# Kernel tuning notes

Hardware: AMD Instinct MI355X
Metric: run time of the kernel (lower is better)

Reference implementation:

```python
import jax, jax.numpy as jnp
import numpy as np
import math

NH = 12  # num_attention_heads (multiple of 4 required by pattern dispatch)


def _forward(Input, hidden_states, attention_mask, Wq, bq, Wk, bk, Wv, bv, Wo, bo, L):
    b, n, _, H = Input.shape
    hd = H // NH
    G = NH // 4  # heads per criss-cross pattern
    # boolean-mask gather of valid (head, tail) entity pairs, row-major like torch
    bi, ri, ci = jnp.nonzero(attention_mask > 0, size=L)
    x = Input[bi, ri, ci]            # [L, H] keys/values source
    xq = hidden_states[bi, ri, ci]   # [L, H] query source
    q = (xq @ Wq + bq).reshape(L, NH, hd)
    k = (x @ Wk + bk).reshape(L, NH, hd)
    v = (x @ Wv + bv).reshape(L, NH, hd)
    ar = jnp.arange(n)
    # per-pattern criss-cross masks for query position (b, r, c), each [L, n]
    m0 = attention_mask[bi, ri, :] * (ar[None, :] != ci[:, None])  # row r, exclude self col c
    m1 = attention_mask[bi, :, ci] * (ar[None, :] != ri[:, None])  # col c, exclude self row r
    m2 = attention_mask[bi, :, ri]                                  # col r (no self exclusion)
    m3 = attention_mask[bi, ci, :]                                  # row c (no self exclusion)
    adds = jnp.stack([(1.0 - m) * -10000.0 for m in (m0, m1, m2, m3)], axis=1)  # [L, 4, n]
    # scatter per-pattern head groups into zero grid, then criss-cross gather
    k_gs, v_gs = [], []
    for p in range(4):
        sk = jnp.zeros((b, n, n, G, hd), k.dtype).at[bi, ri, ci].set(k[:, p::4])
        sv = jnp.zeros((b, n, n, G, hd), v.dtype).at[bi, ri, ci].set(v[:, p::4])
        if p == 0:
            gk, gv = sk[bi, ri], sv[bi, ri]          # element [l,k] = grid[b, r, k]
        elif p == 1:
            gk, gv = sk[bi, :, ci], sv[bi, :, ci]    # grid[b, k, c]
        elif p == 2:
            gk, gv = sk[bi, :, ri], sv[bi, :, ri]    # grid[b, k, r]
        else:
            gk, gv = sk[bi, ci], sv[bi, ci]          # grid[b, c, k]
        k_gs.append(gk)
        v_gs.append(gv)
    kg = jnp.stack(k_gs, axis=1)  # [L, 4, n, G, hd]
    vg = jnp.stack(v_gs, axis=1)
    # head h = 4*g + p (k[:, p::4] picks heads p, p+4, p+8)
    kg = kg.transpose(0, 3, 1, 2, 4).reshape(L, NH, n, hd)
    vg = vg.transpose(0, 3, 1, 2, 4).reshape(L, NH, n, hd)
    amask = jnp.broadcast_to(adds[:, None, :, :], (L, G, 4, n)).reshape(L, NH, n)
    # prepend self key/value; NOTE: original code uses additive bias +1.0 (ones) for the self slot
    kf = jnp.concatenate([k[:, :, None, :], kg], axis=2)   # [L, NH, n+1, hd]
    vf = jnp.concatenate([v[:, :, None, :], vg], axis=2)
    amask = jnp.concatenate([jnp.ones((L, NH, 1), amask.dtype), amask], axis=-1)
    scores = jnp.einsum('lhd,lhkd->lhk', q, kf) / math.sqrt(hd) + amask
    probs = jax.nn.softmax(scores, axis=-1)  # dropout is identity in eval
    ctx = jnp.einsum('lhk,lhkd->lhd', probs, vf).reshape(L, H)
    return ctx @ Wo + bo


def setup_inputs() -> dict:
    key = jax.random.key(0)
    ks = jax.random.split(key, 8)
    b, n, H = 2, 40, 768
    Input = jax.random.normal(ks[0], (b, n, n, H), jnp.float32)
    hidden_states = jax.random.normal(ks[1], (b, n, n, H), jnp.float32)
    # all valid entity pairs except self pairs -> deterministic L
    attention_mask = (jnp.ones((b, n, n)) - jnp.eye(n)[None]).astype(jnp.float32)
    L = int(b * n * (n - 1))  # 3120
    std = 0.02
    Wq = std * jax.random.normal(ks[2], (H, H), jnp.float32)
    Wk = std * jax.random.normal(ks[3], (H, H), jnp.float32)
    Wv = std * jax.random.normal(ks[4], (H, H), jnp.float32)
    Wo = std * jax.random.normal(ks[5], (H, H), jnp.float32)
    bq = jnp.zeros((H,), jnp.float32)
    bk = jnp.zeros((H,), jnp.float32)
    bv = jnp.zeros((H,), jnp.float32)
    bo = jnp.zeros((H,), jnp.float32)
    return {"Input": Input, "hidden_states": hidden_states, "attention_mask": attention_mask,
            "Wq": Wq, "bq": bq, "Wk": Wk, "bk": bk, "Wv": Wv, "bv": bv, "Wo": Wo, "bo": bo, "L": L}


def reference(Input, hidden_states, attention_mask, Wq, bq, Wk, bk, Wv, bv, Wo, bo, L):
    return _forward(Input, hidden_states, attention_mask, Wq, bq, Wk, bk, Wv, bv, Wo, bo, L)
```

## Files before the change

### kernel.cpp

```cpp
#include <hip/hip_runtime.h>
#include <hip/hip_bf16.h>
#include <math.h>

#define NHEADS 12

typedef __attribute__((ext_vector_type(4))) float f32x4;
typedef __attribute__((ext_vector_type(8))) short bf16x8;

__device__ __forceinline__ unsigned short f2bf(float x) {
  __hip_bfloat16 h = __float2bfloat16(x);
  return *reinterpret_cast<unsigned short*>(&h);
}
__device__ __forceinline__ float bf2f(unsigned short u) {
  union { unsigned int i; float f; } c; c.i = ((unsigned int)u) << 16; return c.f;
}

__global__ __launch_bounds__(1024) void build_idx(const float* __restrict__ mask,
                                                  int total,
                                                  int* __restrict__ pos2l,
                                                  int* __restrict__ lidx,
                                                  const float* __restrict__ bk,
                                                  const float* __restrict__ bv,
                                                  float* __restrict__ bkv,
                                                  int H) {
  __shared__ int cnt[1024];
  int t = threadIdx.x;
  if (t < H) { bkv[t] = bk[t]; bkv[H + t] = bv[t]; }
  int per = (total + 1023) >> 10;
  int begin = t * per;
  int end = begin + per; if (end > total) end = total;
  if (begin > total) begin = total;
  int c = 0;
  for (int i = begin; i < end; ++i) c += (mask[i] > 0.f) ? 1 : 0;
  cnt[t] = c;
  __syncthreads();
  for (int off = 1; off < 1024; off <<= 1) {
    int vv = (t >= off) ? cnt[t - off] : 0;
    __syncthreads();
    cnt[t] += vv;
    __syncthreads();
  }
  int excl = cnt[t] - c;
  for (int i = begin; i < end; ++i) {
    if (mask[i] > 0.f) { pos2l[i] = excl; lidx[excl] = i; ++excl; }
    else pos2l[i] = -1;
  }
}

__global__ __launch_bounds__(256) void wconv(const float* __restrict__ W0, const float* __restrict__ W1,
                                             const float* __restrict__ W2, const float* __restrict__ W3,
                                             unsigned short* __restrict__ T0, unsigned short* __restrict__ T1,
                                             unsigned short* __restrict__ T2, unsigned short* __restrict__ T3,
                                             int H) {
  const float* W = (blockIdx.z == 0) ? W0 : (blockIdx.z == 1) ? W1 : (blockIdx.z == 2) ? W2 : W3;
  unsigned short* T = (blockIdx.z == 0) ? T0 : (blockIdx.z == 1) ? T1 : (blockIdx.z == 2) ? T2 : T3;
  __shared__ float tile[32][33];
  int k0 = blockIdx.y * 32, n0 = blockIdx.x * 32;
  int t = threadIdx.x;
  int kk = t >> 3, n4 = (t & 7) * 4;
  float4 v = *reinterpret_cast<const float4*>(W + (size_t)(k0 + kk) * H + n0 + n4);
  tile[n4 + 0][kk] = v.x; tile[n4 + 1][kk] = v.y; tile[n4 + 2][kk] = v.z; tile[n4 + 3][kk] = v.w;
  __syncthreads();
  int nn2 = t >> 3, k4 = (t & 7) * 4;
#pragma unroll
  for (int e = 0; e < 4; ++e)
    T[(size_t)(n0 + nn2) * H + k0 + k4 + e] = f2bf(tile[nn2][k4 + e]);
}

__global__ __launch_bounds__(256) void gatherconv(const float* __restrict__ hidden,
                                                  const float* __restrict__ input,
                                                  const int* __restrict__ lidx,
                                                  unsigned short* __restrict__ Aq,
                                                  unsigned short* __restrict__ Akv,
                                                  int L, int H) {
  int i = blockIdx.x * 256 + threadIdx.x;
  int per = H / 8;
  if (i >= L * per) return;
  int row = i / per;
  int sub = (i - row * per) * 8;
  size_t src = (size_t)lidx[row] * H + sub;
  size_t dst = (size_t)row * H + sub;
  {
    float4 a = *reinterpret_cast<const float4*>(hidden + src);
    float4 b = *reinterpret_cast<const float4*>(hidden + src + 4);
    bf16x8 st;
    st[0]=f2bf(a.x); st[1]=f2bf(a.y); st[2]=f2bf(a.z); st[3]=f2bf(a.w);
    st[4]=f2bf(b.x); st[5]=f2bf(b.y); st[6]=f2bf(b.z); st[7]=f2bf(b.w);
    *reinterpret_cast<bf16x8*>(Aq + dst) = st;
  }
  {
    float4 a = *reinterpret_cast<const float4*>(input + src);
    float4 b = *reinterpret_cast<const float4*>(input + src + 4);
    bf16x8 st;
    st[0]=f2bf(a.x); st[1]=f2bf(a.y); st[2]=f2bf(a.z); st[3]=f2bf(a.w);
    st[4]=f2bf(b.x); st[5]=f2bf(b.y); st[6]=f2bf(b.z); st[7]=f2bf(b.w);
    *reinterpret_cast<bf16x8*>(Akv + dst) = st;
  }
}

#define GBM 128
#define GBN 64
#define GBK 64

template <bool OUT_BF16>
__global__ __launch_bounds__(256) void gemm_bf16(const unsigned short* __restrict__ A,
                                                 const unsigned short* __restrict__ Bt,
                                                 const float* __restrict__ bias,
                                                 void* __restrict__ C,
                                                 int M, int N, int K) {
  __shared__ unsigned short sA[GBM * GBK];
  __shared__ unsigned short sB[GBN * GBK];
  int tid = threadIdx.x;
  int wid = tid >> 6, lane = tid & 63;
  int wm = wid >> 1, wn = wid & 1;
  int m0 = blockIdx.y * GBM, n0 = blockIdx.x * GBN;
  int lr = lane & 15, lq = lane >> 4;
  f32x4 acc[4][2] = {};

  for (int k0 = 0; k0 < K; k0 += GBK) {
#pragma unroll
    for (int r = 0; r < 4; ++r) {
      int c = (r * 4 + wid) * 64 + lane;
      int row = c >> 3, sl = c & 7;
      int sg = sl ^ (row & 7);
      const unsigned short* g = A + (size_t)(m0 + row) * K + k0 + sg * 8;
      __builtin_amdgcn_global_load_lds((const __attribute__((address_space(1))) unsigned int*)g,
                                       (__attribute__((address_space(3))) unsigned int*)(sA + (size_t)(r * 4 + wid) * 512),
                                       16, 0, 0);
    }
#pragma unroll
    for (int r = 0; r < 2; ++r) {
      int c = (r * 4 + wid) * 64 + lane;
      int row = c >> 3, sl = c & 7;
      int sg = sl ^ (row & 7);
      const unsigned short* g = Bt + (size_t)(n0 + row) * K + k0 + sg * 8;
      __builtin_amdgcn_global_load_lds((const __attribute__((address_space(1))) unsigned int*)g,
                                       (__attribute__((address_space(3))) unsigned int*)(sB + (size_t)(r * 4 + wid) * 512),
                                       16, 0, 0);
    }
    __syncthreads();
#pragma unroll
    for (int ks = 0; ks < 2; ++ks) {
      bf16x8 af[4], bfr[2];
#pragma unroll
      for (int i = 0; i < 4; ++i) {
        int row = wm * 64 + i * 16 + lr;
        int slot = (ks * 4 + lq) ^ (row & 7);
        af[i] = *reinterpret_cast<const bf16x8*>(sA + row * 64 + slot * 8);
      }
#pragma unroll
      for (int j = 0; j < 2; ++j) {
        int rn = wn * 32 + j * 16 + lr;
        int slot = (ks * 4 + lq) ^ (rn & 7);
        bfr[j] = *reinterpret_cast<const bf16x8*>(sB + rn * 64 + slot * 8);
      }
#pragma unroll
      for (int i = 0; i < 4; ++i)
#pragma unroll
        for (int j = 0; j < 2; ++j)
          acc[i][j] = __builtin_amdgcn_mfma_f32_16x16x32_bf16(af[i], bfr[j], acc[i][j], 0, 0, 0);
    }
    __syncthreads();
  }

#pragma unroll
  for (int i = 0; i < 4; ++i) {
#pragma unroll
    for (int j = 0; j < 2; ++j) {
      int gcol = n0 + wn * 32 + j * 16 + lr;
      float bv = bias[gcol];
      int rbase = m0 + wm * 64 + i * 16 + lq * 4;
#pragma unroll
      for (int r = 0; r < 4; ++r) {
        int gm = rbase + r;
        if (gm >= M) continue;
        float val = acc[i][j][r] + bv;
        if (OUT_BF16) ((unsigned short*)C)[(size_t)gm * N + gcol] = f2bf(val);
        else          ((float*)C)[(size_t)gm * N + gcol] = val;
      }
    }
  }
}

__global__ __launch_bounds__(128) void attn3(const unsigned short* __restrict__ qb,
                                             const unsigned short* __restrict__ KVb,
                                             const float* __restrict__ mask,
                                             const int* __restrict__ pos2l,
                                             unsigned short* __restrict__ ctx,
                                             int n, int H) {
  __shared__ unsigned short Ks[40 * 72];
  __shared__ unsigned short Vs[40 * 72];
  __shared__ float S[40][42];
  __shared__ float mrow[40];
  __shared__ int qlist[40];

  int bx = blockIdx.x;
  int r0 = bx % n;
  int h3 = (bx / n) % 3;
  int p = (bx / (3 * n)) % 4;
  int bi = bx / (12 * n);
  int h = p + 4 * h3;
  int nn = n * n;
  bool rowkeys = (p == 0 || p == 3);
  bool rowq = (p == 0 || p == 2);
  bool excl = (p < 2);
  int t = threadIdx.x;
  int H2 = 2 * H;

  if (t < 80) {
    int half = t / 40, j = t % 40;
    int keypos = rowkeys ? (r0 * n + j) : (j * n + r0);
    int l2 = pos2l[bi * nn + keypos];
    unsigned short* dst = (half ? Vs : Ks) + j * 72;
    if (l2 >= 0) {
      const unsigned short* src = KVb + (size_t)l2 * H2 + half * H + h * 64;
#pragma unroll
      for (int e8 = 0; e8 < 8; ++e8)
        *reinterpret_cast<bf16x8*>(dst + e8 * 8) = *reinterpret_cast<const bf16x8*>(src + e8 * 8);
    } else {
      bf16x8 z = {};
#pragma unroll
      for (int e8 = 0; e8 < 8; ++e8) *reinterpret_cast<bf16x8*>(dst + e8 * 8) = z;
    }
  }
  if (t < 40) {
    mrow[t] = rowkeys ? mask[bi * nn + r0 * n + t] : mask[bi * nn + t * n + r0];
    int qpos = rowq ? (r0 * n + t) : (t * n + r0);
    qlist[t] = pos2l[bi * nn + qpos];
  }
  __syncthreads();

  int c = t % 40;
  int role = t / 40;
  int lq = (t < 80) ? qlist[c] : -1;

  if (lq >= 0) {
    float qf[64];
    const unsigned short* qp = qb + (size_t)lq * H + h * 64;
#pragma unroll
    for (int e8 = 0; e8 < 8; ++e8) {
      bf16x8 t8 = *reinterpret_cast<const bf16x8*>(qp + e8 * 8);
#pragma unroll
      for (int e = 0; e < 8; ++e) qf[e8 * 8 + e] = bf2f((unsigned short)t8[e]);
    }
    int j0 = role * 20;
#pragma unroll 2
    for (int j = j0; j < j0 + 20; ++j) {
      float acc = 0.f;
#pragma unroll
      for (int e8 = 0; e8 < 8; ++e8) {
        bf16x8 kv = *reinterpret_cast<const bf16x8*>(Ks + j * 72 + e8 * 8);
#pragma unroll
        for (int e = 0; e < 8; ++e) acc = fmaf(qf[e8 * 8 + e], bf2f((unsigned short)kv[e]), acc);
      }
      float mval = mrow[j] * ((excl && j == c) ? 0.f : 1.f);
      S[c][j] = acc * 0.125f + (1.f - mval) * -10000.f;
    }
    if (role == 0) {
      const unsigned short* kp = KVb + (size_t)lq * H2 + h * 64;
      float acc = 0.f;
#pragma unroll
      for (int e8 = 0; e8 < 8; ++e8) {
        bf16x8 kv = *reinterpret_cast<const bf16x8*>(kp + e8 * 8);
#pragma unroll
        for (int e = 0; e < 8; ++e) acc = fmaf(qf[e8 * 8 + e], bf2f((unsigned short)kv[e]), acc);
      }
      S[c][40] = acc * 0.125f + 1.0f;
    }
  }
  __syncthreads();

  if (t < 40 && qlist[t] >= 0) {
    float mx = -3.0e38f;
    for (int j = 0; j <= 40; ++j) mx = fmaxf(mx, S[t][j]);
    float sum = 0.f;
    for (int j = 0; j <= 40; ++j) { float e = __expf(S[t][j] - mx); S[t][j] = e; sum += e; }
    float inv = 1.f / sum;
    for (int j = 0; j <= 40; ++j) S[t][j] *= inv;
  }
  __syncthreads();

  if (lq >= 0) {
    int d0 = role * 32;
    const unsigned short* vsp = KVb + (size_t)lq * H2 + H + h * 64 + d0;
    float pself = S[c][40];
#pragma unroll
    for (int ch = 0; ch < 4; ++ch) {
      int dd = d0 + ch * 8;
      float facc[8];
      bf16x8 vself = *reinterpret_cast<const bf16x8*>(vsp + ch * 8);
#pragma unroll
      for (int e = 0; e < 8; ++e) facc[e] = pself * bf2f((unsigned short)vself[e]);
      for (int j = 0; j < 40; ++j) {
        float pj = S[c][j];
        bf16x8 vv = *reinterpret_cast<const bf16x8*>(Vs + j * 72 + dd);
#pragma unroll
        for (int e = 0; e < 8; ++e) facc[e] = fmaf(pj, bf2f((unsigned short)vv[e]), facc[e]);
      }
      bf16x8 st;
#pragma unroll
      for (int e = 0; e < 8; ++e) st[e] = f2bf(facc[e]);
      *reinterpret_cast<bf16x8*>(ctx + (size_t)lq * H + h * 64 + dd) = st;
    }
  }
}

extern "C" void kernel_launch(void* const* d_in, const int* in_sizes, int n_in,
                              void* d_out, int out_size, void* d_ws, size_t ws_size,
                              hipStream_t stream) {
  const float* Input  = (const float*)d_in[0];
  const float* hidden = (const float*)d_in[1];
  const float* mask   = (const float*)d_in[2];
  const float* Wq = (const float*)d_in[3];
  const float* bq = (const float*)d_in[4];
  const float* Wk = (const float*)d_in[5];
  const float* bk = (const float*)d_in[6];
  const float* Wv = (const float*)d_in[7];
  const float* bv = (const float*)d_in[8];
  const float* Wo = (const float*)d_in[9];
  const float* bo = (const float*)d_in[10];

  int H = (int)llround(sqrt((double)in_sizes[3]));
  int total = in_sizes[2];
  int L = out_size / H;
  int bn = total - L;
  int n = total / bn;
  int b = bn / n;
  int mtiles = (L + GBM - 1) / GBM;
  int Mpad = mtiles * GBM;
  size_t aElems = (size_t)Mpad * H;

  char* p = (char*)d_ws;
  auto take = [&](size_t bytes) { char* r = p; p += (bytes + 255) & ~(size_t)255; return r; };
  int* lidx  = (int*)take((size_t)L * 4);
  int* pos2l = (int*)take((size_t)total * 4);
  float* bkv = (float*)take((size_t)2 * H * 4);
  unsigned short* Wqt  = (unsigned short*)take((size_t)H * H * 2);
  unsigned short* Wot  = (unsigned short*)take((size_t)H * H * 2);
  unsigned short* Wkvt = (unsigned short*)take((size_t)2 * H * H * 2);
  unsigned short* Aq   = (unsigned short*)take(aElems * 2);
  unsigned short* Akv  = (unsigned short*)take(aElems * 2);
  unsigned short* qb2  = (unsigned short*)take(aElems * 2);
  unsigned short* KVb  = (unsigned short*)take(aElems * 2 * 2);
  unsigned short* ctxb = (unsigned short*)take(aElems * 2);

  build_idx<<<1, 1024, 0, stream>>>(mask, total, pos2l, lidx, bk, bv, bkv, H);
  wconv<<<dim3(H / 32, H / 32, 4), 256, 0, stream>>>(Wq, Wk, Wv, Wo, Wqt, Wkvt, Wkvt + (size_t)H * H, Wot, H);
  {
    int nthr = L * (H / 8);
    gatherconv<<<(nthr + 255) / 256, 256, 0, stream>>>(hidden, Input, lidx, Aq, Akv, L, H);
  }
  gemm_bf16<true><<<dim3(H / GBN, mtiles), 256, 0, stream>>>(Aq,  Wqt,  bq,  qb2, L, H,     H);
  gemm_bf16<true><<<dim3(2 * H / GBN, mtiles), 256, 0, stream>>>(Akv, Wkvt, bkv, KVb, L, 2 * H, H);
  attn3<<<b * 4 * 3 * n, 128, 0, stream>>>(qb2, KVb, mask, pos2l, ctxb, n, H);
  gemm_bf16<false><<<dim3(H / GBN, mtiles), 256, 0, stream>>>(ctxb, Wot, bo, (float*)d_out, L, H, H);
}
```

Baseline: 96.69 us.

## Merge prep kernels, fuse Q and KV GEMMs, double-buffer GEMM LDS staging

Folds the index-build and weight-conversion kernels into one launch, with a single trailing block doing the mask scan on 256 threads instead of 1024. The Q and KV projections are merged into one GEMM launch that picks its operands by block index. The GEMM core now double-buffers LDS so the next K tile is loaded while MFMAs run on the current one, dropping one barrier per iteration. This cuts launch count and hides global-load latency, at the cost of twice the LDS per block (possibly lower occupancy) and a slower serial scan in the prep block.

```diff
diff --git a/kernel.cpp b/kernel.cpp
--- a/kernel.cpp
+++ b/kernel.cpp
@@ -15,56 +15,59 @@
   union { unsigned int i; float f; } c; c.i = ((unsigned int)u) << 16; return c.f;
 }
 
-__global__ __launch_bounds__(1024) void build_idx(const float* __restrict__ mask,
-                                                  int total,
-                                                  int* __restrict__ pos2l,
-                                                  int* __restrict__ lidx,
-                                                  const float* __restrict__ bk,
-                                                  const float* __restrict__ bv,
-                                                  float* __restrict__ bkv,
-                                                  int H) {
-  __shared__ int cnt[1024];
+__global__ __launch_bounds__(256) void prep(const float* __restrict__ mask, int total,
+                                            int* __restrict__ pos2l, int* __restrict__ lidx,
+                                            const float* __restrict__ bk, const float* __restrict__ bv,
+                                            float* __restrict__ bkv,
+                                            const float* __restrict__ W0, const float* __restrict__ W1,
+                                            const float* __restrict__ W2, const float* __restrict__ W3,
+                                            unsigned short* __restrict__ T0, unsigned short* __restrict__ T1,
+                                            unsigned short* __restrict__ T2, unsigned short* __restrict__ T3,
+                                            int H) {
+  int nt32 = H / 32;
+  int nw = nt32 * nt32 * 4;
+  int bx = blockIdx.x;
   int t = threadIdx.x;
-  if (t < H) { bkv[t] = bk[t]; bkv[H + t] = bv[t]; }
-  int per = (total + 1023) >> 10;
-  int begin = t * per;
-  int end = begin + per; if (end > total) end = total;
-  if (begin > total) begin = total;
-  int c = 0;
-  for (int i = begin; i < end; ++i) c += (mask[i] > 0.f) ? 1 : 0;
-  cnt[t] = c;
-  __syncthreads();
-  for (int off = 1; off < 1024; off <<= 1) {
-    int vv = (t >= off) ? cnt[t - off] : 0;
+  if (bx < nw) {
+    __shared__ float tile[32][33];
+    int z = bx / (nt32 * nt32);
+    int rem = bx - z * nt32 * nt32;
+    int byy = rem / nt32;
+    int bxx = rem - byy * nt32;
+    const float* W = (z == 0) ? W0 : (z == 1) ? W1 : (z == 2) ? W2 : W3;
+    unsigned short* T = (z == 0) ? T0 : (z == 1) ? T1 : (z == 2) ? T2 : T3;
+    int k0 = byy * 32, n0 = bxx * 32;
+    int kk = t >> 3, n4 = (t & 7) * 4;
+    float4 v = *reinterpret_cast<const float4*>(W + (size_t)(k0 + kk) * H + n0 + n4);
+    tile[n4 + 0][kk] = v.x; tile[n4 + 1][kk] = v.y; tile[n4 + 2][kk] = v.z; tile[n4 + 3][kk] = v.w;
     __syncthreads();
-    cnt[t] += vv;
+    int nn2 = t >> 3, k4 = (t & 7) * 4;
+#pragma unroll
+    for (int e = 0; e < 4; ++e)
+      T[(size_t)(n0 + nn2) * H + k0 + k4 + e] = f2bf(tile[nn2][k4 + e]);
+  } else {
+    __shared__ int cnt[256];
+    for (int i = t; i < H; i += 256) { bkv[i] = bk[i]; bkv[H + i] = bv[i]; }
+    int per = (total + 255) >> 8;
+    int begin = t * per;
+    int end = begin + per; if (end > total) end = total;
+    if (begin > total) begin = total;
+    int c = 0;
+    for (int i = begin; i < end; ++i) c += (mask[i] > 0.f) ? 1 : 0;
+    cnt[t] = c;
     __syncthreads();
-  }
-  int excl = cnt[t] - c;
-  for (int i = begin; i < end; ++i) {
-    if (mask[i] > 0.f) { pos2l[i] = excl; lidx[excl] = i; ++excl; }
-    else pos2l[i] = -1;
-  }
-}
-
-__global__ __launch_bounds__(256) void wconv(const float* __restrict__ W0, const float* __restrict__ W1,
-                                             const float* __restrict__ W2, const float* __restrict__ W3,
-                                             unsigned short* __restrict__ T0, unsigned short* __restrict__ T1,
-                                             unsigned short* __restrict__ T2, unsigned short* __restrict__ T3,
-                                             int H) {
-  const float* W = (blockIdx.z == 0) ? W0 : (blockIdx.z == 1) ? W1 : (blockIdx.z == 2) ? W2 : W3;
-  unsigned short* T = (blockIdx.z == 0) ? T0 : (blockIdx.z == 1) ? T1 : (blockIdx.z == 2) ? T2 : T3;
-  __shared__ float tile[32][33];
-  int k0 = blockIdx.y * 32, n0 = blockIdx.x * 32;
-  int t = threadIdx.x;
-  int kk = t >> 3, n4 = (t & 7) * 4;
-  float4 v = *reinterpret_cast<const float4*>(W + (size_t)(k0 + kk) * H + n0 + n4);
-  tile[n4 + 0][kk] = v.x; tile[n4 + 1][kk] = v.y; tile[n4 + 2][kk] = v.z; tile[n4 + 3][kk] = v.w;
-  __syncthreads();
-  int nn2 = t >> 3, k4 = (t & 7) * 4;
-#pragma unroll
-  for (int e = 0; e < 4; ++e)
-    T[(size_t)(n0 + nn2) * H + k0 + k4 + e] = f2bf(tile[nn2][k4 + e]);
+    for (int off = 1; off < 256; off <<= 1) {
+      int vv = (t >= off) ? cnt[t - off] : 0;
+      __syncthreads();
+      cnt[t] += vv;
+      __syncthreads();
+    }
+    int excl = cnt[t] - c;
+    for (int i = begin; i < end; ++i) {
+      if (mask[i] > 0.f) { pos2l[i] = excl; lidx[excl] = i; ++excl; }
+      else pos2l[i] = -1;
+    }
+  }
 }
 
 __global__ __launch_bounds__(256) void gatherconv(const float* __restrict__ hidden,
@@ -103,21 +106,19 @@
 #define GBK 64
 
 template <bool OUT_BF16>
-__global__ __launch_bounds__(256) void gemm_bf16(const unsigned short* __restrict__ A,
-                                                 const unsigned short* __restrict__ Bt,
-                                                 const float* __restrict__ bias,
-                                                 void* __restrict__ C,
-                                                 int M, int N, int K) {
-  __shared__ unsigned short sA[GBM * GBK];
-  __shared__ unsigned short sB[GBN * GBK];
+__device__ __forceinline__ void gemm_core(const unsigned short* __restrict__ A,
+                                          const unsigned short* __restrict__ Bt,
+                                          const float* __restrict__ bias,
+                                          void* __restrict__ C,
+                                          int M, int N, int K, int m0, int n0,
+                                          unsigned short* sA, unsigned short* sB) {
   int tid = threadIdx.x;
   int wid = tid >> 6, lane = tid & 63;
   int wm = wid >> 1, wn = wid & 1;
-  int m0 = blockIdx.y * GBM, n0 = blockIdx.x * GBN;
   int lr = lane & 15, lq = lane >> 4;
   f32x4 acc[4][2] = {};
 
-  for (int k0 = 0; k0 < K; k0 += GBK) {
+  auto STAGE = [&](int buf, int k0) {
 #pragma unroll
     for (int r = 0; r < 4; ++r) {
       int c = (r * 4 + wid) * 64 + lane;
@@ -125,7 +126,7 @@
       int sg = sl ^ (row & 7);
       const unsigned short* g = A + (size_t)(m0 + row) * K + k0 + sg * 8;
       __builtin_amdgcn_global_load_lds((const __attribute__((address_space(1))) unsigned int*)g,
-                                       (__attribute__((address_space(3))) unsigned int*)(sA + (size_t)(r * 4 + wid) * 512),
+                                       (__attribute__((address_space(3))) unsigned int*)(sA + buf * (GBM * GBK) + (r * 4 + wid) * 512),
                                        16, 0, 0);
     }
 #pragma unroll
@@ -135,10 +136,19 @@
       int sg = sl ^ (row & 7);
       const unsigned short* g = Bt + (size_t)(n0 + row) * K + k0 + sg * 8;
       __builtin_amdgcn_global_load_lds((const __attribute__((address_space(1))) unsigned int*)g,
-                                       (__attribute__((address_space(3))) unsigned int*)(sB + (size_t)(r * 4 + wid) * 512),
+                                       (__attribute__((address_space(3))) unsigned int*)(sB + buf * (GBN * GBK) + (r * 4 + wid) * 512),
                                        16, 0, 0);
     }
+  };
+
+  const int nt = K / GBK;
+  STAGE(0, 0);
+  int cur = 0;
+  for (int t = 0; t < nt; ++t) {
     __syncthreads();
+    if (t + 1 < nt) STAGE(cur ^ 1, (t + 1) * GBK);
+    const unsigned short* pA = sA + cur * (GBM * GBK);
+    const unsigned short* pB = sB + cur * (GBN * GBK);
 #pragma unroll
     for (int ks = 0; ks < 2; ++ks) {
       bf16x8 af[4], bfr[2];
@@ -146,13 +156,13 @@
       for (int i = 0; i < 4; ++i) {
         int row = wm * 64 + i * 16 + lr;
         int slot = (ks * 4 + lq) ^ (row & 7);
-        af[i] = *reinterpret_cast<const bf16x8*>(sA + row * 64 + slot * 8);
+        af[i] = *reinterpret_cast<const bf16x8*>(pA + row * 64 + slot * 8);
       }
 #pragma unroll
       for (int j = 0; j < 2; ++j) {
         int rn = wn * 32 + j * 16 + lr;
         int slot = (ks * 4 + lq) ^ (rn & 7);
-        bfr[j] = *reinterpret_cast<const bf16x8*>(sB + rn * 64 + slot * 8);
+        bfr[j] = *reinterpret_cast<const bf16x8*>(pB + rn * 64 + slot * 8);
       }
 #pragma unroll
       for (int i = 0; i < 4; ++i)
@@ -160,7 +170,7 @@
         for (int j = 0; j < 2; ++j)
           acc[i][j] = __builtin_amdgcn_mfma_f32_16x16x32_bf16(af[i], bfr[j], acc[i][j], 0, 0, 0);
     }
-    __syncthreads();
+    cur ^= 1;
   }
 
 #pragma unroll
@@ -180,6 +190,36 @@
       }
     }
   }
+}
+
+__global__ __launch_bounds__(256) void gemm_qkv(const unsigned short* __restrict__ Aq,
+                                                const unsigned short* __restrict__ Akv,
+                                                const unsigned short* __restrict__ Wqt,
+                                                const unsigned short* __restrict__ Wkvt,
+                                                const float* __restrict__ bq,
+                                                const float* __restrict__ bkv,
+                                                unsigned short* __restrict__ Cq,
+                                                unsigned short* __restrict__ Ckv,
+                                                int M, int K, int H) {
+  __shared__ unsigned short sA[2 * GBM * GBK];
+  __shared__ unsigned short sB[2 * GBN * GBK];
+  int nq = H / GBN;
+  int bx = blockIdx.x;
+  int m0 = blockIdx.y * GBM;
+  if (bx < nq)
+    gemm_core<true>(Aq, Wqt, bq, Cq, M, H, K, m0, bx * GBN, sA, sB);
+  else
+    gemm_core<true>(Akv, Wkvt, bkv, Ckv, M, 2 * H, K, m0, (bx - nq) * GBN, sA, sB);
+}
+
+__global__ __launch_bounds__(256) void gemm_out(const unsigned short* __restrict__ A,
+                                                const unsigned short* __restrict__ Bt,
+                                                const float* __restrict__ bias,
+                                                float* __restrict__ C,
+                                                int M, int N, int K) {
+  __shared__ unsigned short sA[2 * GBM * GBK];
+  __shared__ unsigned short sB[2 * GBN * GBK];
+  gemm_core<false>(A, Bt, bias, C, M, N, K, blockIdx.y * GBM, blockIdx.x * GBN, sA, sB);
 }
 
 __global__ __launch_bounds__(128) void attn3(const unsigned short* __restrict__ qb,
@@ -344,14 +384,17 @@
   unsigned short* KVb  = (unsigned short*)take(aElems * 2 * 2);
   unsigned short* ctxb = (unsigned short*)take(aElems * 2);
 
-  build_idx<<<1, 1024, 0, stream>>>(mask, total, pos2l, lidx, bk, bv, bkv, H);
-  wconv<<<dim3(H / 32, H / 32, 4), 256, 0, stream>>>(Wq, Wk, Wv, Wo, Wqt, Wkvt, Wkvt + (size_t)H * H, Wot, H);
+  int nt32 = H / 32;
+  int nwconv = nt32 * nt32 * 4;
+  prep<<<nwconv + 1, 256, 0, stream>>>(mask, total, pos2l, lidx, bk, bv, bkv,
+                                       Wq, Wk, Wv, Wo,
+                                       Wqt, Wkvt, Wkvt + (size_t)H * H, Wot, H);
   {
     int nthr = L * (H / 8);
     gatherconv<<<(nthr + 255) / 256, 256, 0, stream>>>(hidden, Input, lidx, Aq, Akv, L, H);
   }
-  gemm_bf16<true><<<dim3(H / GBN, mtiles), 256, 0, stream>>>(Aq,  Wqt,  bq,  qb2, L, H,     H);
-  gemm_bf16<true><<<dim3(2 * H / GBN, mtiles), 256, 0, stream>>>(Akv, Wkvt, bkv, KVb, L, 2 * H, H);
+  gemm_qkv<<<dim3(3 * H / GBN, mtiles), 256, 0, stream>>>(Aq, Akv, Wqt, Wkvt, bq, bkv,
+                                                          qb2, KVb, L, H, H);
   attn3<<<b * 4 * 3 * n, 128, 0, stream>>>(qb2, KVb, mask, pos2l, ctxb, n, H);
-  gemm_bf16<false><<<dim3(H / GBN, mtiles), 256, 0, stream>>>(ctxb, Wot, bo, (float*)d_out, L, H, H);
-}
+  gemm_out<<<dim3(H / GBN, mtiles), 256, 0, stream>>>(ctxb, Wot, bo, (float*)d_out, L, H, H);
+}
```

After: 99.35 us. 2.7% more time.
